# Kernel optimization log

Measured on AMD Instinct MI355X. Metric: run time of the kernel, lower is better.

Reference implementation:

```python
import jax, jax.numpy as jnp
import numpy as np

B, T, D, H, FC, A = 256, 128, 512, 1024, 1024, 32
LOG_STD_MIN, LOG_STD_MAX = -20.0, 2.0
EPS = 1e-5


def setup_inputs() -> dict:
    key = jax.random.key(0)
    ks = jax.random.split(key, 16)
    def w(k, shape, fan_in):
        return jax.random.normal(k, shape, jnp.float32) / np.float32(np.sqrt(fan_in))
    return {
        "observations": jax.random.normal(ks[0], (B, T, D), jnp.float32),
        "hidden_state": jax.random.normal(ks[1], (B, H), jnp.float32),
        "episode_starts": jax.random.randint(ks[2], (B, T), 0, 2, jnp.int32),
        "ln_gamma": jnp.ones((D,), jnp.float32),
        "ln_beta": jnp.zeros((D,), jnp.float32),
        "W_fc": w(ks[3], (FC, D), D), "b_fc": jnp.zeros((FC,), jnp.float32),
        "W_ih": w(ks[4], (3 * H, FC), FC), "b_ih": jnp.zeros((3 * H,), jnp.float32),
        "W_hh": w(ks[5], (3 * H, H), H), "b_hh": jnp.zeros((3 * H,), jnp.float32),
        "W_out": w(ks[6], (H, H), H), "b_out": jnp.zeros((H,), jnp.float32),
        "W_mean": w(ks[7], (A, H), H) * 0.01, "b_mean": jnp.zeros((A,), jnp.float32),
        "W_ls": w(ks[8], (A, H), H) * 0.01, "b_ls": jnp.zeros((A,), jnp.float32),
    }


def reference(observations, hidden_state, episode_starts, ln_gamma, ln_beta,
              W_fc, b_fc, W_ih, b_ih, W_hh, b_hh, W_out, b_out,
              W_mean, b_mean, W_ls, b_ls):
    # LayerNorm over last dim (eps=1e-5, like nn.LayerNorm)
    mu = jnp.mean(observations, axis=-1, keepdims=True)
    var = jnp.mean(jnp.square(observations - mu), axis=-1, keepdims=True)
    x = (observations - mu) * jax.lax.rsqrt(var + EPS) * ln_gamma + ln_beta
    # fc_in + ReLU, then precompute GRU input-gate projections for all steps
    x = jax.nn.relu(jnp.einsum('btd,fd->btf', x, W_fc) + b_fc)          # (B,T,FC)
    xg = jnp.einsum('btf,gf->btg', x, W_ih) + b_ih                      # (B,T,3H)
    xg_t = jnp.swapaxes(xg, 0, 1)                                       # (T,B,3H)
    starts_t = jnp.swapaxes(episode_starts, 0, 1).astype(jnp.float32)   # (T,B)

    def step(h, inp):
        xg_s, st = inp
        h = h * (1.0 - st)[:, None]
        gh = h @ W_hh.T + b_hh                                           # (B,3H)
        xr, xz, xn = xg_s[:, :H], xg_s[:, H:2 * H], xg_s[:, 2 * H:]
        hr, hz, hn = gh[:, :H], gh[:, H:2 * H], gh[:, 2 * H:]
        r = jax.nn.sigmoid(xr + hr)
        z = jax.nn.sigmoid(xz + hz)
        n = jnp.tanh(xn + r * hn)
        h_new = (1.0 - z) * n + z * h
        out = jax.nn.relu(h_new @ W_out.T + b_out)
        return h_new, out

    h_final, outs = jax.lax.scan(step, hidden_state, (xg_t, starts_t))
    feats = jnp.swapaxes(outs, 0, 1)                                     # (B,T,H)
    means = jnp.einsum('bth,ah->bta', feats, W_mean) + b_mean
    log_std = jnp.clip(jnp.einsum('bth,ah->bta', feats, W_ls) + b_ls,
                       LOG_STD_MIN, LOG_STD_MAX)
    return means, log_std, h_final
```

## Files before the change

### kernel.cpp

```cpp
#include <hip/hip_runtime.h>
#include <hip/hip_bf16.h>

#define B_ 256
#define T_ 128
#define D_ 512
#define H_ 1024
#define FC_ 1024
#define A_ 32
#define NWG_ 256

typedef short bf16x8 __attribute__((ext_vector_type(8)));
typedef float f32x4 __attribute__((ext_vector_type(4)));
typedef unsigned long long ull;
typedef ull ullx2 __attribute__((ext_vector_type(2)));

__device__ __forceinline__ float bf2f(unsigned short u) {
  return __uint_as_float(((unsigned)u) << 16);
}
__device__ __forceinline__ unsigned short f2bf(float x) {
  unsigned u = __float_as_uint(x);
  u = u + 0x7fffu + ((u >> 16) & 1u);
  return (unsigned short)(u >> 16);
}
__device__ __forceinline__ void unpack8(uint4 v, float* f) {
  f[0] = bf2f(v.x & 0xffff); f[1] = bf2f(v.x >> 16);
  f[2] = bf2f(v.y & 0xffff); f[3] = bf2f(v.y >> 16);
  f[4] = bf2f(v.z & 0xffff); f[5] = bf2f(v.z >> 16);
  f[6] = bf2f(v.w & 0xffff); f[7] = bf2f(v.w >> 16);
}
__device__ __forceinline__ uint4 pack8(const float* f) {
  uint4 v;
  v.x = (unsigned)f2bf(f[0]) | ((unsigned)f2bf(f[1]) << 16);
  v.y = (unsigned)f2bf(f[2]) | ((unsigned)f2bf(f[3]) << 16);
  v.z = (unsigned)f2bf(f[4]) | ((unsigned)f2bf(f[5]) << 16);
  v.w = (unsigned)f2bf(f[6]) | ((unsigned)f2bf(f[7]) << 16);
  return v;
}

__global__ __launch_bounds__(256) void detect_kernel(
    const unsigned short* __restrict__ obs, int* __restrict__ flag)
{
  __shared__ int cnt;
  if (threadIdx.x == 0) cnt = 0;
  __syncthreads();
  int c = 0;
  for (int i = threadIdx.x; i < 8192; i += 256) {
    unsigned e = (obs[i] >> 7) & 0xffu;
    if (e >= 0x86u) c++;
  }
  atomicAdd(&cnt, c);
  __syncthreads();
  if (threadIdx.x == 0) *flag = (cnt >= 64) ? 1 : 0;
}

struct CanonArgs {
  const void* src[14];
  unsigned short* dst[14];
  int ofs[15];
};
__global__ __launch_bounds__(256) void canon_kernel(CanonArgs a,
                                                    const int* __restrict__ flag)
{
  const int fl = *flag;
  const int i0 = (blockIdx.x * 256 + threadIdx.x) * 8;
  int t = 0;
  while (t < 14 && i0 >= a.ofs[t + 1]) t++;
  if (t >= 14) return;
  const int local = i0 - a.ofs[t];
  unsigned short* d = a.dst[t] + local;
  if (fl) {
    const float* s = (const float*)a.src[t] + local;
    #pragma unroll
    for (int e = 0; e < 8; e++) d[e] = f2bf(s[e]);
  } else {
    const unsigned short* s = (const unsigned short*)a.src[t] + local;
    #pragma unroll
    for (int e = 0; e < 8; e++) d[e] = s[e];
  }
}

__global__ __launch_bounds__(256) void ln_kernel(
    const void* __restrict__ obs,
    const unsigned short* __restrict__ gamma_,
    const unsigned short* __restrict__ beta_,
    unsigned short* __restrict__ xn, int t0, int tcShift,
    const int* __restrict__ flag)
{
  const int fl = *flag;
  const int lane = threadIdx.x & 63;
  const int rloc = blockIdx.x * 4 + (threadIdx.x >> 6);
  const int b  = rloc >> tcShift;
  const int tl = rloc & ((1 << tcShift) - 1);
  const int grow = b * T_ + t0 + tl;
  float f[8];
  if (fl) {
    const float* of = (const float*)obs + (size_t)grow * D_ + lane * 8;
    const float4 v0 = *(const float4*)of;
    const float4 v1 = *(const float4*)(of + 4);
    f[0] = v0.x; f[1] = v0.y; f[2] = v0.z; f[3] = v0.w;
    f[4] = v1.x; f[5] = v1.y; f[6] = v1.z; f[7] = v1.w;
  } else {
    uint4 v = *(const uint4*)((const unsigned short*)obs + (size_t)grow * D_ + lane * 8);
    unpack8(v, f);
  }
  float s = 0.f, ss = 0.f;
  #pragma unroll
  for (int i = 0; i < 8; i++) { s += f[i]; ss += f[i] * f[i]; }
  #pragma unroll
  for (int off = 32; off > 0; off >>= 1) {
    s  += __shfl_xor(s,  off, 64);
    ss += __shfl_xor(ss, off, 64);
  }
  const float mu  = s * (1.0f / D_);
  const float var = ss * (1.0f / D_) - mu * mu;
  const float inv = rsqrtf(var + 1e-5f);
  float g[8], b8[8];
  unpack8(*(const uint4*)(gamma_ + lane * 8), g);
  unpack8(*(const uint4*)(beta_  + lane * 8), b8);
  float o[8];
  #pragma unroll
  for (int i = 0; i < 8; i++) o[i] = (f[i] - mu) * inv * g[i] + b8[i];
  *(uint4*)(xn + (size_t)rloc * D_ + lane * 8) = pack8(o);
}

__global__ __launch_bounds__(256) void gemm_tn(
    const unsigned short* __restrict__ A, const unsigned short* __restrict__ Bm,
    const unsigned short* __restrict__ bias, unsigned short* __restrict__ C,
    int M, int N, int K, int relu)
{
  __shared__ short As[128 * 32];
  __shared__ short Bs[128 * 32];
  const int tid  = threadIdx.x;
  const int wave = tid >> 6, lane = tid & 63;
  const int quad = lane >> 4, l15 = lane & 15;
  const int m0 = blockIdx.y * 128, n0 = blockIdx.x * 128;
  const int wm = (wave >> 1) * 64, wn = (wave & 1) * 64;
  const int srow = tid >> 2;
  const int skc  = (tid & 3) * 8;
  const size_t aoff0 = (size_t)(m0 + srow) * K + skc;
  const size_t aoff1 = (size_t)(m0 + 64 + srow) * K + skc;
  const size_t boff0 = (size_t)(n0 + srow) * K + skc;
  const size_t boff1 = (size_t)(n0 + 64 + srow) * K + skc;
  const int lb0 = wave * 512;
  const int lb1 = 2048 + wave * 512;
  f32x4 acc[4][4] = {};
  for (int k0 = 0; k0 < K; k0 += 32) {
    __syncthreads();
    __builtin_amdgcn_global_load_lds(
        (const __attribute__((address_space(1))) unsigned*)(A + aoff0 + k0),
        (__attribute__((address_space(3))) unsigned*)&As[lb0], 16, 0, 0);
    __builtin_amdgcn_global_load_lds(
        (const __attribute__((address_space(1))) unsigned*)(A + aoff1 + k0),
        (__attribute__((address_space(3))) unsigned*)&As[lb1], 16, 0, 0);
    __builtin_amdgcn_global_load_lds(
        (const __attribute__((address_space(1))) unsigned*)(Bm + boff0 + k0),
        (__attribute__((address_space(3))) unsigned*)&Bs[lb0], 16, 0, 0);
    __builtin_amdgcn_global_load_lds(
        (const __attribute__((address_space(1))) unsigned*)(Bm + boff1 + k0),
        (__attribute__((address_space(3))) unsigned*)&Bs[lb1], 16, 0, 0);
    __syncthreads();
    bf16x8 af[4], bfv[4];
    #pragma unroll
    for (int i = 0; i < 4; i++) af[i]  = *(const bf16x8*)&As[(wm + i * 16 + l15) * 32 + quad * 8];
    #pragma unroll
    for (int j = 0; j < 4; j++) bfv[j] = *(const bf16x8*)&Bs[(wn + j * 16 + l15) * 32 + quad * 8];
    #pragma unroll
    for (int i = 0; i < 4; i++)
      #pragma unroll
      for (int j = 0; j < 4; j++)
        acc[i][j] = __builtin_amdgcn_mfma_f32_16x16x32_bf16(af[i], bfv[j], acc[i][j], 0, 0, 0);
  }
  #pragma unroll
  for (int j = 0; j < 4; j++) {
    const int col = n0 + wn + j * 16 + l15;
    const float bj = bias ? bf2f(bias[col]) : 0.0f;
    #pragma unroll
    for (int i = 0; i < 4; i++) {
      const int row = m0 + wm + i * 16 + quad * 4;
      #pragma unroll
      for (int r = 0; r < 4; r++) {
        float v = acc[i][j][r] + bj;
        if (relu) v = fmaxf(v, 0.0f);
        C[(size_t)(row + r) * N + col] = f2bf(v);
      }
    }
  }
}

__global__ __launch_bounds__(256, 1) void gru_scan(
    const unsigned short* __restrict__ xg,
    const int* __restrict__ starts,
    const unsigned short* __restrict__ Whh,
    const unsigned short* __restrict__ bhh,
    float* __restrict__ hf,
    ull* __restrict__ hb0,
    ull* __restrict__ hb1,
    unsigned short* __restrict__ hall,
    int t0, int Tc,
    int* __restrict__ flags)
{
  __shared__ short Ws[3 * 16 * 1032];
  __shared__ short Hs[4 * 2 * 2176];
  __shared__ unsigned sbits[64][4];
  const int tid  = threadIdx.x;
  const int wg   = blockIdx.x;
  const int jb   = wg & 63, bb = wg >> 6;
  const int j0   = jb * 16, b0 = bb * 64;
  const int wave = tid >> 6, lane = tid & 63;
  const int quad = lane >> 4, l15 = lane & 15;
  const int quad2 = quad * 2;

  for (int c = tid; c < 48 * 128; c += 256) {
    const int row = c >> 7;
    const int kc  = (c & 127) * 8;
    const int g = row >> 4, jj = row & 15;
    *(uint4*)&Ws[row * 1032 + kc] =
        *(const uint4*)(Whh + (size_t)(g * H_ + j0 + jj) * H_ + kc);
  }
  for (int c = tid; c < 64 * 4; c += 256) {
    const int row = c >> 2, w = c & 3;
    unsigned m = 0;
    #pragma unroll
    for (int bi = 0; bi < 32; bi++)
      m |= (starts[(b0 + row) * T_ + w * 32 + bi] ? 1u : 0u) << bi;
    sbits[row][w] = m;
  }
  const float br = bf2f(bhh[j0 + l15]);
  const float bz = bf2f(bhh[H_ + j0 + l15]);
  const float bn = bf2f(bhh[2 * H_ + j0 + l15]);
  const int col = j0 + l15;

  const int r0 = wave * 16 + quad * 4;
  float hreg[4];
  #pragma unroll
  for (int r = 0; r < 4; r++)
    hreg[r] = hf[(size_t)(b0 + r0 + r) * H_ + col];

  const int arow = wave * 16 + l15;
  const size_t hrowbase = ((size_t)(b0 + arow)) << 8;
  const short* wsb = &Ws[l15 * 1032 + quad * 8];
  const int hsbase = wave * 4352 + l15 * 136 + quad * 8;

  __syncthreads();

#define GRU_LOADC(dst, c)                                                     \
  { _Pragma("unroll")                                                         \
    for (int w4 = 0; w4 < 4; w4++) {                                          \
      dst[2 * w4]     = __hip_atomic_load(hp + (c) * 32 + w4 * 8 + quad2,     \
                          __ATOMIC_RELAXED, __HIP_MEMORY_SCOPE_AGENT);        \
      dst[2 * w4 + 1] = __hip_atomic_load(hp + (c) * 32 + w4 * 8 + quad2 + 1, \
                          __ATOMIC_RELAXED, __HIP_MEMORY_SCOPE_AGENT);        \
    } }

#define GRU_SM(src, c)                                                        \
  { _Pragma("unroll")                                                         \
    for (int w4 = 0; w4 < 4; w4++) {                                          \
      ullx2 u2;                                                               \
      u2.x = src[2 * w4] & keep;                                              \
      u2.y = src[2 * w4 + 1] & keep;                                          \
      *(uint4*)&Hs[hsbase + ((c) & 1) * 2176 + w4 * 32] =                     \
          __builtin_bit_cast(uint4, u2);                                      \
    }                                                                         \
    _Pragma("unroll")                                                         \
    for (int w4 = 0; w4 < 4; w4++) {                                          \
      const bf16x8 a =                                                        \
          *(const bf16x8*)&Hs[hsbase + ((c) & 1) * 2176 + w4 * 32];           \
      acc[0] = __builtin_amdgcn_mfma_f32_16x16x32_bf16(                       \
          a, *(const bf16x8*)(wsb + 0 * 16512 + ((c) * 4 + w4) * 32),         \
          acc[0], 0, 0, 0);                                                   \
      acc[1] = __builtin_amdgcn_mfma_f32_16x16x32_bf16(                       \
          a, *(const bf16x8*)(wsb + 1 * 16512 + ((c) * 4 + w4) * 32),         \
          acc[1], 0, 0, 0);                                                   \
      acc[2] = __builtin_amdgcn_mfma_f32_16x16x32_bf16(                       \
          a, *(const bf16x8*)(wsb + 2 * 16512 + ((c) * 4 + w4) * 32),         \
          acc[2], 0, 0, 0);                                                   \
    } }

  for (int tl = 0; tl < Tc; tl++) {
    const int t = t0 + tl;
    const ull* hin = (t & 1) ? hb1 : hb0;
    unsigned* hout_u = (unsigned*)((t & 1) ? hb0 : hb1);
    const unsigned tw = (unsigned)(t >> 5), tb = (unsigned)(t & 31);
    const ull* hp = hin + hrowbase;

    ull pf0[8], pf1[8], pf2[8];
    GRU_LOADC(pf0, 0)
    GRU_LOADC(pf1, 1)
    GRU_LOADC(pf2, 2)

    float xr[4], xz[4], xnv[4];
    #pragma unroll
    for (int r = 0; r < 4; r++) {
      const size_t xrow = ((size_t)(b0 + r0 + r) * Tc + tl) * (3 * H_);
      xr[r]  = bf2f(xg[xrow + col]);
      xz[r]  = bf2f(xg[xrow + H_ + col]);
      xnv[r] = bf2f(xg[xrow + 2 * H_ + col]);
    }

    const ull keep = ((sbits[arow][tw] >> tb) & 1u) ? 0ull : ~0ull;

    f32x4 acc[3] = {};
    GRU_SM(pf0, 0) GRU_LOADC(pf0, 3)
    GRU_SM(pf1, 1) GRU_LOADC(pf1, 4)
    GRU_SM(pf2, 2) GRU_LOADC(pf2, 5)
    GRU_SM(pf0, 3) GRU_LOADC(pf0, 6)
    GRU_SM(pf1, 4) GRU_LOADC(pf1, 7)
    GRU_SM(pf2, 5)
    GRU_SM(pf0, 6)
    GRU_SM(pf1, 7)

    #pragma unroll
    for (int r = 0; r < 4; r++) {
      const int lrow = r0 + r;
      const int b = b0 + lrow;
      const float kb = ((sbits[lrow][tw] >> tb) & 1u) ? 0.0f : 1.0f;
      const float hr = acc[0][r] + br;
      const float hz = acc[1][r] + bz;
      const float hn = acc[2][r] + bn;
      const float rg = 1.0f / (1.0f + __expf(-(xr[r] + hr)));
      const float zg = 1.0f / (1.0f + __expf(-(xz[r] + hz)));
      const float ng = tanhf(xnv[r] + rg * hn);
      const float hv = (1.0f - zg) * ng + zg * (hreg[r] * kb);
      hreg[r] = hv;
      const unsigned mine = (unsigned)f2bf(hv);
      const unsigned other = (unsigned)__shfl_xor((int)mine, 1, 64);
      if ((l15 & 1) == 0) {
        const unsigned packed = mine | (other << 16);
        __hip_atomic_store(&hout_u[((size_t)b * H_ + col) >> 1], packed,
                           __ATOMIC_RELAXED, __HIP_MEMORY_SCOPE_AGENT);
        ((unsigned*)hall)[(((size_t)b * Tc + tl) * H_ + col) >> 1] = packed;
      }
    }

    const int my = t0 + tl + 1;
    __builtin_amdgcn_s_waitcnt(0);
    __syncthreads();
    if (tid == 0)
      __hip_atomic_store(&flags[wg * 32], my, __ATOMIC_RELAXED,
                         __HIP_MEMORY_SCOPE_AGENT);
    if (tid < 64) {
      while (__hip_atomic_load(&flags[(bb * 64 + tid) * 32], __ATOMIC_RELAXED,
                               __HIP_MEMORY_SCOPE_AGENT) < my)
        __builtin_amdgcn_s_sleep(1);
    }
    __syncthreads();
  }
#undef GRU_LOADC
#undef GRU_SM

  #pragma unroll
  for (int r = 0; r < 4; r++)
    hf[(size_t)(b0 + r0 + r) * H_ + col] = hreg[r];
}

__global__ __launch_bounds__(256) void heads_kernel(
    const unsigned short* __restrict__ feats,
    const unsigned short* __restrict__ Wm, const unsigned short* __restrict__ bm,
    const unsigned short* __restrict__ Wl, const unsigned short* __restrict__ bl,
    void* __restrict__ outbuf, int t0, int tcShift, const int* __restrict__ flag)
{
  __shared__ short Fs[64][40];
  __shared__ short Ws[64][40];
  const int fl = *flag;
  const int tid  = threadIdx.x;
  const int wave = tid >> 6, lane = tid & 63;
  const int quad = lane >> 4, l15 = lane & 15;
  const int m0 = blockIdx.x * 64;
  const int lrow = tid >> 2, lk = (tid & 3) * 8;
  f32x4 acc[4] = {};
  for (int k0 = 0; k0 < H_; k0 += 32) {
    __syncthreads();
    *(uint4*)&Fs[lrow][lk] = *(const uint4*)(feats + (size_t)(m0 + lrow) * H_ + k0 + lk);
    const unsigned short* wsrc = (lrow < 32)
        ? (Wm + (size_t)lrow * H_ + k0 + lk)
        : (Wl + (size_t)(lrow - 32) * H_ + k0 + lk);
    *(uint4*)&Ws[lrow][lk] = *(const uint4*)wsrc;
    __syncthreads();
    bf16x8 af = *(const bf16x8*)&Fs[wave * 16 + l15][quad * 8];
    #pragma unroll
    for (int j = 0; j < 4; j++) {
      bf16x8 bfv = *(const bf16x8*)&Ws[j * 16 + l15][quad * 8];
      acc[j] = __builtin_amdgcn_mfma_f32_16x16x32_bf16(af, bfv, acc[j], 0, 0, 0);
    }
  }
  const int tcMask = (1 << tcShift) - 1;
  const size_t lstdBase = (size_t)B_ * T_ * A_;
  #pragma unroll
  for (int j = 0; j < 4; j++) {
    const int col = j * 16 + l15;
    #pragma unroll
    for (int r = 0; r < 4; r++) {
      const int row = m0 + wave * 16 + quad * 4 + r;
      const int grow = (row >> tcShift) * T_ + t0 + (row & tcMask);
      float v = acc[j][r];
      size_t idx;
      if (col < 32) {
        v += bf2f(bm[col]);
        idx = (size_t)grow * A_ + col;
      } else {
        v += bf2f(bl[col - 32]);
        v = fminf(fmaxf(v, -20.0f), 2.0f);
        idx = lstdBase + (size_t)grow * A_ + (col - 32);
      }
      if (fl) ((float*)outbuf)[idx] = v;
      else    ((unsigned short*)outbuf)[idx] = f2bf(v);
    }
  }
}

__global__ __launch_bounds__(256) void h0_cast(const void* __restrict__ h0,
                                               float* __restrict__ hf,
                                               unsigned short* __restrict__ hb0,
                                               const int* __restrict__ flag) {
  const int fl = *flag;
  int i = blockIdx.x * 256 + threadIdx.x;
  float v = fl ? ((const float*)h0)[i] : bf2f(((const unsigned short*)h0)[i]);
  hf[i] = v;
  hb0[i] = f2bf(v);
}
__global__ __launch_bounds__(256) void hfin_store(const float* __restrict__ h,
                                                  void* __restrict__ outbuf,
                                                  const int* __restrict__ flag) {
  const int fl = *flag;
  const size_t base = 2ull * B_ * T_ * A_;
  int i = blockIdx.x * 256 + threadIdx.x;
  if (fl) ((float*)outbuf)[base + i] = h[i];
  else    ((unsigned short*)outbuf)[base + i] = f2bf(h[i]);
}

extern "C" void kernel_launch(void* const* d_in, const int* in_sizes, int n_in,
                              void* d_out, int out_size, void* d_ws, size_t ws_size,
                              hipStream_t stream)
{
  const void* obs    = d_in[0];
  const void* h0in   = d_in[1];
  const int*  starts = (const int*)d_in[2];
  const void* fsrc[14] = { d_in[5], d_in[7], d_in[9], d_in[11], d_in[13], d_in[15],
                           d_in[3], d_in[4], d_in[6], d_in[8], d_in[10], d_in[12],
                           d_in[14], d_in[16] };
  const int fn[14] = { FC_ * D_, 3 * H_ * FC_, 3 * H_ * H_, H_ * H_, A_ * H_, A_ * H_,
                       D_, D_, FC_, 3 * H_, 3 * H_, H_, A_, A_ };

  char* ws = (char*)d_ws;
  int* flag = (int*)ws;
  size_t cur = 256;
  unsigned short* cdst[14];
  for (int i = 0; i < 14; i++) {
    cdst[i] = (unsigned short*)(ws + cur);
    cur += (size_t)fn[i] * 2;
    cur = (cur + 255) & ~255ull;
  }
  const size_t chunkBase = cur;
  const size_t fixedTail = 1048576ull  + 2ull * 524288ull
                         + 32768ull ;

  int Tc = 1;
  for (int c = 32; c >= 1; c >>= 1) {
    size_t need = chunkBase + (size_t)c * 2883584ull + fixedTail;
    if (need <= ws_size) { Tc = c; break; }
  }
  int tcShift = 0;
  while ((1 << tcShift) < Tc) tcShift++;

  unsigned short* xn   = (unsigned short*)(ws + chunkBase);
  unsigned short* xfc  = (unsigned short*)(ws + chunkBase + (size_t)Tc * 262144ull);
  unsigned short* xg   = (unsigned short*)(ws + chunkBase + (size_t)Tc * 786432ull);
  unsigned short* hall = (unsigned short*)(ws + chunkBase + (size_t)Tc * 2359296ull);
  size_t o = chunkBase + (size_t)Tc * 2883584ull;
  float* hf           = (float*)(ws + o);           o += 1048576ull;
  unsigned short* hb0 = (unsigned short*)(ws + o);  o += 524288ull;
  unsigned short* hb1 = (unsigned short*)(ws + o);  o += 524288ull;
  int* flags          = (int*)(ws + o);
  unsigned short* feats = xg;

  const unsigned short *Wfc = cdst[0], *Wih = cdst[1], *Whh = cdst[2], *Wout = cdst[3];
  const unsigned short *Wmean = cdst[4], *Wls = cdst[5];
  const unsigned short *gam = cdst[6], *bet = cdst[7], *bfc = cdst[8], *bih = cdst[9];
  const unsigned short *bhh = cdst[10], *bout = cdst[11], *bmean = cdst[12], *bls = cdst[13];

  detect_kernel<<<dim3(1), dim3(256), 0, stream>>>((const unsigned short*)obs, flag);
  CanonArgs ca;
  int total = 0;
  for (int i = 0; i < 14; i++) {
    ca.src[i] = fsrc[i];
    ca.dst[i] = cdst[i];
    ca.ofs[i] = total;
    total += fn[i];
  }
  ca.ofs[14] = total;
  canon_kernel<<<dim3((total / 8 + 255) / 256), dim3(256), 0, stream>>>(ca, flag);
  h0_cast<<<dim3(B_ * H_ / 256), dim3(256), 0, stream>>>(h0in, hf, hb0, flag);
  hipMemsetAsync(flags, 0, 32768, stream);

  const int Mc = B_ * Tc;
  for (int t0 = 0; t0 < T_; t0 += Tc) {
    ln_kernel<<<dim3(Mc / 4), dim3(256), 0, stream>>>(obs, gam, bet, xn, t0, tcShift, flag);
    gemm_tn<<<dim3(FC_ / 128, Mc / 128), dim3(256), 0, stream>>>(
        xn, Wfc, bfc, xfc, Mc, FC_, D_, 1);
    gemm_tn<<<dim3(3 * H_ / 128, Mc / 128), dim3(256), 0, stream>>>(
        xfc, Wih, bih, xg, Mc, 3 * H_, FC_, 0);

    gru_scan<<<dim3(NWG_), dim3(256), 0, stream>>>(
        xg, starts, Whh, bhh, hf,
        (ull*)hb0, (ull*)hb1,
        hall, t0, Tc, flags);

    gemm_tn<<<dim3(H_ / 128, Mc / 128), dim3(256), 0, stream>>>(
        hall, Wout, bout, feats, Mc, H_, H_, 1);
    heads_kernel<<<dim3(Mc / 64), dim3(256), 0, stream>>>(
        feats, Wmean, bmean, Wls, bls, d_out, t0, tcShift, flag);
  }

  hfin_store<<<dim3(B_ * H_ / 256), dim3(256), 0, stream>>>(hf, d_out, flag);
}
```

Measured before the change: 2.126 ms.

## Share hidden-state loads across waves via block-wide LDS staging in GRU scan

Before this change, each wave loaded its own 16 rows of the previous hidden state from global memory into private LDS slots. Now the whole 256-thread block loads the 64x1024 hidden tile cooperatively with coalesced 8-byte atomic loads, applies the episode-start mask per row, and writes it into a shared double-chunk LDS buffer that all waves read for their MFMAs. The intent is better coalescing and fewer redundant global loads per step. The cost is eight extra block-wide barriers per timestep and shallower prefetch (two chunks instead of three), which may serialize load and compute.

```diff
diff --git a/kernel.cpp b/kernel.cpp
--- a/kernel.cpp
+++ b/kernel.cpp
@@ -12,7 +12,6 @@
 typedef short bf16x8 __attribute__((ext_vector_type(8)));
 typedef float f32x4 __attribute__((ext_vector_type(4)));
 typedef unsigned long long ull;
-typedef ull ullx2 __attribute__((ext_vector_type(2)));
 
 __device__ __forceinline__ float bf2f(unsigned short u) {
   return __uint_as_float(((unsigned)u) << 16);
@@ -200,7 +199,7 @@
     int* __restrict__ flags)
 {
   __shared__ short Ws[3 * 16 * 1032];
-  __shared__ short Hs[4 * 2 * 2176];
+  __shared__ short Hs[2 * 64 * 136];
   __shared__ unsigned sbits[64][4];
   const int tid  = threadIdx.x;
   const int wg   = blockIdx.x;
@@ -208,7 +207,6 @@
   const int j0   = jb * 16, b0 = bb * 64;
   const int wave = tid >> 6, lane = tid & 63;
   const int quad = lane >> 4, l15 = lane & 15;
-  const int quad2 = quad * 2;
 
   for (int c = tid; c < 48 * 128; c += 256) {
     const int row = c >> 7;
@@ -236,43 +234,54 @@
   for (int r = 0; r < 4; r++)
     hreg[r] = hf[(size_t)(b0 + r0 + r) * H_ + col];
 
-  const int arow = wave * 16 + l15;
-  const size_t hrowbase = ((size_t)(b0 + arow)) << 8;
+  const int srow0 = tid >> 5;
+  const int scol  = tid & 31;
+  const size_t hbg = (size_t)(b0 + srow0) * 256 + scol;
+  const int hsW = srow0 * 136 + scol * 4;
+  const int hsR = (wave * 16 + l15) * 136 + quad * 8;
   const short* wsb = &Ws[l15 * 1032 + quad * 8];
-  const int hsbase = wave * 4352 + l15 * 136 + quad * 8;
 
   __syncthreads();
 
-#define GRU_LOADC(dst, c)                                                     \
+#define GRU_LOADC(dst, ch)                                                    \
+  { _Pragma("unroll")                                                         \
+    for (int u = 0; u < 8; u++)                                               \
+      dst[u] = __hip_atomic_load(hin + hbg + u * 2048 + (ch) * 32,            \
+                                 __ATOMIC_RELAXED, __HIP_MEMORY_SCOPE_AGENT); }
+
+#define GRU_WRITE(src, s)                                                     \
+  { _Pragma("unroll")                                                         \
+    for (int u = 0; u < 8; u++) {                                             \
+      ull v = src[u];                                                         \
+      if ((sbits[srow0 + u * 8][tw] >> tb) & 1u) v = 0ull;                    \
+      *(ull*)&Hs[(s) * 8704 + hsW + u * 1088] = v;                            \
+    } }
+
+#define GRU_MFMA2(p)                                                          \
   { _Pragma("unroll")                                                         \
     for (int w4 = 0; w4 < 4; w4++) {                                          \
-      dst[2 * w4]     = __hip_atomic_load(hp + (c) * 32 + w4 * 8 + quad2,     \
-                          __ATOMIC_RELAXED, __HIP_MEMORY_SCOPE_AGENT);        \
-      dst[2 * w4 + 1] = __hip_atomic_load(hp + (c) * 32 + w4 * 8 + quad2 + 1, \
-                          __ATOMIC_RELAXED, __HIP_MEMORY_SCOPE_AGENT);        \
-    } }
-
-#define GRU_SM(src, c)                                                        \
-  { _Pragma("unroll")                                                         \
-    for (int w4 = 0; w4 < 4; w4++) {                                          \
-      ullx2 u2;                                                               \
-      u2.x = src[2 * w4] & keep;                                              \
-      u2.y = src[2 * w4 + 1] & keep;                                          \
-      *(uint4*)&Hs[hsbase + ((c) & 1) * 2176 + w4 * 32] =                     \
-          __builtin_bit_cast(uint4, u2);                                      \
+      const bf16x8 a = *(const bf16x8*)&Hs[hsR + w4 * 32];                    \
+      acc[0] = __builtin_amdgcn_mfma_f32_16x16x32_bf16(                       \
+          a, *(const bf16x8*)(wsb + 0 * 16512 + ((2*(p))*4 + w4) * 32),       \
+          acc[0], 0, 0, 0);                                                   \
+      acc[1] = __builtin_amdgcn_mfma_f32_16x16x32_bf16(                       \
+          a, *(const bf16x8*)(wsb + 1 * 16512 + ((2*(p))*4 + w4) * 32),       \
+          acc[1], 0, 0, 0);                                                   \
+      acc[2] = __builtin_amdgcn_mfma_f32_16x16x32_bf16(                       \
+          a, *(const bf16x8*)(wsb + 2 * 16512 + ((2*(p))*4 + w4) * 32),       \
+          acc[2], 0, 0, 0);                                                   \
     }                                                                         \
     _Pragma("unroll")                                                         \
     for (int w4 = 0; w4 < 4; w4++) {                                          \
-      const bf16x8 a =                                                        \
-          *(const bf16x8*)&Hs[hsbase + ((c) & 1) * 2176 + w4 * 32];           \
+      const bf16x8 a = *(const bf16x8*)&Hs[8704 + hsR + w4 * 32];             \
       acc[0] = __builtin_amdgcn_mfma_f32_16x16x32_bf16(                       \
-          a, *(const bf16x8*)(wsb + 0 * 16512 + ((c) * 4 + w4) * 32),         \
+          a, *(const bf16x8*)(wsb + 0 * 16512 + ((2*(p)+1)*4 + w4) * 32),     \
           acc[0], 0, 0, 0);                                                   \
       acc[1] = __builtin_amdgcn_mfma_f32_16x16x32_bf16(                       \
-          a, *(const bf16x8*)(wsb + 1 * 16512 + ((c) * 4 + w4) * 32),         \
+          a, *(const bf16x8*)(wsb + 1 * 16512 + ((2*(p)+1)*4 + w4) * 32),     \
           acc[1], 0, 0, 0);                                                   \
       acc[2] = __builtin_amdgcn_mfma_f32_16x16x32_bf16(                       \
-          a, *(const bf16x8*)(wsb + 2 * 16512 + ((c) * 4 + w4) * 32),         \
+          a, *(const bf16x8*)(wsb + 2 * 16512 + ((2*(p)+1)*4 + w4) * 32),     \
           acc[2], 0, 0, 0);                                                   \
     } }
 
@@ -281,12 +290,10 @@
     const ull* hin = (t & 1) ? hb1 : hb0;
     unsigned* hout_u = (unsigned*)((t & 1) ? hb0 : hb1);
     const unsigned tw = (unsigned)(t >> 5), tb = (unsigned)(t & 31);
-    const ull* hp = hin + hrowbase;
-
-    ull pf0[8], pf1[8], pf2[8];
+
+    ull pf0[8], pf1[8];
     GRU_LOADC(pf0, 0)
     GRU_LOADC(pf1, 1)
-    GRU_LOADC(pf2, 2)
 
     float xr[4], xz[4], xnv[4];
     #pragma unroll
@@ -297,17 +304,26 @@
       xnv[r] = bf2f(xg[xrow + 2 * H_ + col]);
     }
 
-    const ull keep = ((sbits[arow][tw] >> tb) & 1u) ? 0ull : ~0ull;
-
     f32x4 acc[3] = {};
-    GRU_SM(pf0, 0) GRU_LOADC(pf0, 3)
-    GRU_SM(pf1, 1) GRU_LOADC(pf1, 4)
-    GRU_SM(pf2, 2) GRU_LOADC(pf2, 5)
-    GRU_SM(pf0, 3) GRU_LOADC(pf0, 6)
-    GRU_SM(pf1, 4) GRU_LOADC(pf1, 7)
-    GRU_SM(pf2, 5)
-    GRU_SM(pf0, 6)
-    GRU_SM(pf1, 7)
+    __syncthreads();
+    GRU_WRITE(pf0, 0) GRU_WRITE(pf1, 1)
+    __syncthreads();
+    GRU_LOADC(pf0, 2) GRU_LOADC(pf1, 3)
+    GRU_MFMA2(0)
+    __syncthreads();
+    GRU_WRITE(pf0, 0) GRU_WRITE(pf1, 1)
+    __syncthreads();
+    GRU_LOADC(pf0, 4) GRU_LOADC(pf1, 5)
+    GRU_MFMA2(1)
+    __syncthreads();
+    GRU_WRITE(pf0, 0) GRU_WRITE(pf1, 1)
+    __syncthreads();
+    GRU_LOADC(pf0, 6) GRU_LOADC(pf1, 7)
+    GRU_MFMA2(2)
+    __syncthreads();
+    GRU_WRITE(pf0, 0) GRU_WRITE(pf1, 1)
+    __syncthreads();
+    GRU_MFMA2(3)
 
     #pragma unroll
     for (int r = 0; r < 4; r++) {
@@ -346,7 +362,8 @@
     __syncthreads();
   }
 #undef GRU_LOADC
-#undef GRU_SM
+#undef GRU_WRITE
+#undef GRU_MFMA2
 
   #pragma unroll
   for (int r = 0; r < 4; r++)
```

Measured after the change: 1.784 ms. 16.1% less time.
